# Optimization experiments

Hardware: AMD Instinct MI355X
Metric: run time of the kernel (lower is better)

## Reference

```python
import jax, jax.numpy as jnp
import numpy as np

H = 8  # num_heads
EPS = 1e-5

def _layernorm(x, g, b):
    mu = jnp.mean(x, axis=-1, keepdims=True)
    var = jnp.var(x, axis=-1, keepdims=True)
    return (x - mu) * jax.lax.rsqrt(var + EPS) * g + b

def setup_inputs() -> dict:
    key = jax.random.key(0)
    ks = jax.random.split(key, 16)
    B, S, D, F = 1, 4096, 512, 2048
    s = 1.0 / np.sqrt(D)
    inp = {
        'x': jax.random.normal(ks[0], (B, S, D), jnp.float32),
        'mask': jax.random.randint(ks[1], (S, S), 0, 2, jnp.int32),
        'wq': jax.random.normal(ks[2], (D, D), jnp.float32) * s,
        'bq': jnp.zeros((D,), jnp.float32),
        'wk': jax.random.normal(ks[3], (D, D), jnp.float32) * s,
        'bk': jnp.zeros((D,), jnp.float32),
        'wv': jax.random.normal(ks[4], (D, D), jnp.float32) * s,
        'bv': jnp.zeros((D,), jnp.float32),
        'wo': jax.random.normal(ks[5], (D, D), jnp.float32) * s,
        'bo': jnp.zeros((D,), jnp.float32),
        'w1': jax.random.normal(ks[6], (D, F), jnp.float32) * s,
        'b1': jnp.zeros((F,), jnp.float32),
        'w2': jax.random.normal(ks[7], (F, D), jnp.float32) * (1.0 / np.sqrt(F)),
        'b2': jnp.zeros((D,), jnp.float32),
        'g1': jnp.ones((D,), jnp.float32),
        'be1': jnp.zeros((D,), jnp.float32),
        'g2': jnp.ones((D,), jnp.float32),
        'be2': jnp.zeros((D,), jnp.float32),
    }
    return inp

def reference(x, mask, wq, bq, wk, bk, wv, bv, wo, bo, w1, b1, w2, b2, g1, be1, g2, be2):
    B, S, D = x.shape
    Dh = D // H

    def split(t):  # (B,S,D) -> (B,H,S,Dh)
        return t.reshape(B, S, H, Dh).transpose(0, 2, 1, 3)

    q = split(x @ wq + bq)
    k = split(x @ wk + bk)
    v = split(x @ wv + bv)

    # naive attention: full (B,H,S,S) scores, NO 1/sqrt(Dh) scaling (faithful to source)
    scores = jnp.einsum('bhsd,bhtd->bhst', q, k)
    scores = jnp.where(mask == 0, jnp.float32(-1e9), scores)
    attn = jax.nn.softmax(scores, axis=-1)
    out = jnp.einsum('bhst,bhtd->bhsd', attn, v)
    out = out.transpose(0, 2, 1, 3).reshape(B, S, D) @ wo + bo

    x = _layernorm(x + out, g1, be1)  # dropout is identity at inference
    ff = jax.nn.relu(x @ w1 + b1) @ w2 + b2
    x = _layernorm(x + ff, g2, be2)
    return x
```

## Files before the change

kernel.cpp:

```cpp
#include <hip/hip_runtime.h>

typedef unsigned short u16;
typedef unsigned int u32;
typedef unsigned long long u64;
typedef __attribute__((ext_vector_type(4))) float f32x4;
typedef __attribute__((ext_vector_type(8))) short bf16x8;
typedef __attribute__((ext_vector_type(4))) u16 u16x4;
typedef __attribute__((ext_vector_type(2))) u32 u32x2;

#define DEV __device__ __forceinline__

DEV u16 f2bf(float f) {
  union { float f; u32 u; } c; c.f = f;
  u32 u = c.u;
  u += 0x7fffu + ((u >> 16) & 1u);
  return (u16)(u >> 16);
}
DEV float bf2f(u16 h) {
  union { u32 u; float f; } c; c.u = ((u32)h) << 16;
  return c.f;
}
DEV u32 fbits(float f) { union { float f; u32 u; } c; c.f = f; return c.u; }
DEV u32 packtrunc(float a, float b) {
  return (fbits(b) & 0xFFFF0000u) | (fbits(a) >> 16);
}

DEV void gload_lds16(const void* g, void* l) {
  __builtin_amdgcn_global_load_lds(
      (const __attribute__((address_space(1))) u32*)(u64)g,
      (__attribute__((address_space(3))) u32*)(u32)(u64)l,
      16, 0, 0);
}

struct PrepW { const float* w; u16* th; u16* tl; int R, C, gxmask, gxshift; };
struct PrepArgs {
  const float* x; u16* xh; u16* xl;
  const int* mask; unsigned long long* mbits;
  PrepW pw[6];
};

__global__ __launch_bounds__(256) void prep(PrepArgs a) {
  __shared__ float t[32][33];
  int b = blockIdx.x, tid = threadIdx.x;
  if (b < 2048) {
    int i = (b * 256 + tid) * 4;
    f32x4 v = *(const f32x4*)(a.x + i);
    u16x4 h, l;
#pragma unroll
    for (int j = 0; j < 4; ++j) { h[j] = f2bf(v[j]); l[j] = f2bf(v[j] - bf2f(h[j])); }
    *(u16x4*)(a.xh + i) = h;
    *(u16x4*)(a.xl + i) = l;
    return;
  }
  b -= 2048;
  if (b < 3072) {
    int wi, base;
    if (b < 1024) { wi = b >> 8; base = b & 255; }
    else if (b < 2048) { wi = 4; base = b - 1024; }
    else { wi = 5; base = b - 2048; }
    PrepW p = a.pw[wi];
    int c0 = (base & p.gxmask) * 32, r0 = (base >> p.gxshift) * 32;
    int tx = tid & 31, ty = tid >> 5;
#pragma unroll
    for (int i = 0; i < 4; ++i)
      t[ty + 8 * i][tx] = p.w[(size_t)(r0 + ty + 8 * i) * p.C + c0 + tx];
    __syncthreads();
#pragma unroll
    for (int i = 0; i < 4; ++i) {
      float v = t[tx][ty + 8 * i];
      u16 h = f2bf(v);
      size_t o = (size_t)(c0 + ty + 8 * i) * p.R + r0 + tx;
      p.th[o] = h;
      p.tl[o] = f2bf(v - bf2f(h));
    }
    return;
  }
  b -= 3072;
  size_t i = (size_t)b * 256 + tid;
  unsigned long long bb = __ballot(a.mask[i] != 0);
  if ((tid & 63) == 0) a.mbits[i >> 6] = bb;
}

struct QkvArgs {
  const u16 *Ah, *Al;
  const u16 *Bh[3], *Bl[3];
  const float* bias[3];
  u16 *Qh, *Ql, *Kh, *Vt;
};

__global__ __launch_bounds__(256) void gemm_qkv(QkvArgs a) {
  const int K = 512;
  const float L2E = 1.44269504088896340736f;
  const int z = blockIdx.z;
  const u16* __restrict__ Bh = a.Bh[z];
  const u16* __restrict__ Bl = a.Bl[z];
  const float* __restrict__ bias = a.bias[z];
  const int bn = blockIdx.x * 128, bm = blockIdx.y * 128;
  const int tid = threadIdx.x;
  const int wave = tid >> 6, lane = tid & 63;
  const int l16 = lane & 15, quad = lane >> 4;
  const int wm = (wave >> 1) * 64, wn = (wave & 1) * 64;

  __shared__ u16 sA[128 * 32];
  __shared__ u16 sB[128 * 32];
  __shared__ u16 sAl[128 * 32];
  __shared__ u16 sBl[128 * 32];

  const int srow = wave * 32 + (lane >> 2);
  const int scol = (lane & 3) * 8;
  const u16* srcA0 = a.Ah + (size_t)(bm + srow) * K + scol;
  const u16* srcB0 = Bh + (size_t)(bn + srow) * K + scol;
  const u16* srcAl0 = a.Al + (size_t)(bm + srow) * K + scol;
  const u16* srcBl0 = Bl + (size_t)(bn + srow) * K + scol;
  const size_t half_off = (size_t)16 * K;
  u16* dstA = sA + wave * 1024;
  u16* dstB = sB + wave * 1024;
  u16* dstAl = sAl + wave * 1024;
  u16* dstBl = sBl + wave * 1024;

  f32x4 acc[4][4] = {};

  for (int kt = 0; kt < K; kt += 32) {
    gload_lds16(srcA0 + kt, dstA);
    gload_lds16(srcA0 + half_off + kt, dstA + 512);
    gload_lds16(srcB0 + kt, dstB);
    gload_lds16(srcB0 + half_off + kt, dstB + 512);
    gload_lds16(srcAl0 + kt, dstAl);
    gload_lds16(srcAl0 + half_off + kt, dstAl + 512);
    gload_lds16(srcBl0 + kt, dstBl);
    gload_lds16(srcBl0 + half_off + kt, dstBl + 512);
    __syncthreads();

    bf16x8 a_h[4], b_h[4], a_l[4], b_l[4];
#pragma unroll
    for (int mt = 0; mt < 4; ++mt) {
      a_h[mt] = *(const bf16x8*)(sA + (wm + mt * 16 + l16) * 32 + quad * 8);
      a_l[mt] = *(const bf16x8*)(sAl + (wm + mt * 16 + l16) * 32 + quad * 8);
    }
#pragma unroll
    for (int nt = 0; nt < 4; ++nt) {
      b_h[nt] = *(const bf16x8*)(sB + (wn + nt * 16 + l16) * 32 + quad * 8);
      b_l[nt] = *(const bf16x8*)(sBl + (wn + nt * 16 + l16) * 32 + quad * 8);
    }
#pragma unroll
    for (int mt = 0; mt < 4; ++mt)
#pragma unroll
      for (int nt = 0; nt < 4; ++nt) {
        acc[mt][nt] = __builtin_amdgcn_mfma_f32_16x16x32_bf16(a_h[mt], b_h[nt], acc[mt][nt], 0, 0, 0);
        acc[mt][nt] = __builtin_amdgcn_mfma_f32_16x16x32_bf16(a_h[mt], b_l[nt], acc[mt][nt], 0, 0, 0);
        acc[mt][nt] = __builtin_amdgcn_mfma_f32_16x16x32_bf16(a_l[mt], b_h[nt], acc[mt][nt], 0, 0, 0);
      }
    __syncthreads();
  }

  if (z == 2) {
#pragma unroll
    for (int nt = 0; nt < 4; ++nt) {
      int col = bn + wn + nt * 16 + l16;
      float bv = bias[col];
#pragma unroll
      for (int mt = 0; mt < 4; ++mt) {
        int row0 = bm + wm + mt * 16 + quad * 4;
        u16x4 o;
#pragma unroll
        for (int r = 0; r < 4; ++r) o[r] = f2bf(acc[mt][nt][r] + bv);
        *(u16x4*)(a.Vt + (size_t)col * 4096 + row0) = o;
      }
    }
  } else if (z == 0) {
#pragma unroll
    for (int mt = 0; mt < 4; ++mt)
#pragma unroll
      for (int nt = 0; nt < 4; ++nt) {
        int col = bn + wn + nt * 16 + l16;
        float bv = bias[col];
#pragma unroll
        for (int r = 0; r < 4; ++r) {
          int row = bm + wm + mt * 16 + quad * 4 + r;
          float v = (acc[mt][nt][r] + bv) * L2E;
          u16 h = f2bf(v);
          size_t oidx = (size_t)row * 512 + col;
          a.Qh[oidx] = h;
          a.Ql[oidx] = f2bf(v - bf2f(h));
        }
      }
  } else {
#pragma unroll
    for (int mt = 0; mt < 4; ++mt)
#pragma unroll
      for (int nt = 0; nt < 4; ++nt) {
        int col = bn + wn + nt * 16 + l16;
        float bv = bias[col];
#pragma unroll
        for (int r = 0; r < 4; ++r) {
          int row = bm + wm + mt * 16 + quad * 4 + r;
          a.Kh[(size_t)row * 512 + col] = f2bf(acc[mt][nt][r] + bv);
        }
      }
  }
}

template <int RELU, int BF16OUT>
__global__ __launch_bounds__(256) void gemm_bt(const u16* __restrict__ Ah,
                                               const u16* __restrict__ Bh,
                                               const float* __restrict__ bias,
                                               float* __restrict__ Cf,
                                               u16* __restrict__ Ch,
                                               int N, int K) {
  const int bn = blockIdx.x * 128, bm = blockIdx.y * 128;
  const int tid = threadIdx.x;
  const int wave = tid >> 6, lane = tid & 63;
  const int l16 = lane & 15, quad = lane >> 4;
  const int wm = (wave >> 1) * 64, wn = (wave & 1) * 64;

  __shared__ u16 sA[128 * 32];
  __shared__ u16 sB[128 * 32];

  const int srow = wave * 32 + (lane >> 2);
  const int scol = (lane & 3) * 8;
  const u16* srcA0 = Ah + (size_t)(bm + srow) * K + scol;
  const u16* srcB0 = Bh + (size_t)(bn + srow) * K + scol;
  const size_t half_off = (size_t)16 * K;
  u16* dstA = sA + wave * 1024;
  u16* dstB = sB + wave * 1024;

  f32x4 acc[4][4] = {};

  for (int kt = 0; kt < K; kt += 32) {
    gload_lds16(srcA0 + kt, dstA);
    gload_lds16(srcA0 + half_off + kt, dstA + 512);
    gload_lds16(srcB0 + kt, dstB);
    gload_lds16(srcB0 + half_off + kt, dstB + 512);
    __syncthreads();

    bf16x8 a_h[4], b_h[4];
#pragma unroll
    for (int mt = 0; mt < 4; ++mt)
      a_h[mt] = *(const bf16x8*)(sA + (wm + mt * 16 + l16) * 32 + quad * 8);
#pragma unroll
    for (int nt = 0; nt < 4; ++nt)
      b_h[nt] = *(const bf16x8*)(sB + (wn + nt * 16 + l16) * 32 + quad * 8);
#pragma unroll
    for (int mt = 0; mt < 4; ++mt)
#pragma unroll
      for (int nt = 0; nt < 4; ++nt)
        acc[mt][nt] = __builtin_amdgcn_mfma_f32_16x16x32_bf16(a_h[mt], b_h[nt], acc[mt][nt], 0, 0, 0);
    __syncthreads();
  }

#pragma unroll
  for (int mt = 0; mt < 4; ++mt)
#pragma unroll
    for (int nt = 0; nt < 4; ++nt) {
      int col = bn + wn + nt * 16 + l16;
      float bv = bias ? bias[col] : 0.f;
#pragma unroll
      for (int r = 0; r < 4; ++r) {
        int row = bm + wm + mt * 16 + quad * 4 + r;
        float v = acc[mt][nt][r] + bv;
        if (RELU) v = fmaxf(v, 0.f);
        size_t oidx = (size_t)row * N + col;
        if (BF16OUT) Ch[oidx] = f2bf(v);
        else Cf[oidx] = v;
      }
    }
}

__global__ __launch_bounds__(256) void attn(const u16* __restrict__ Qh, const u16* __restrict__ Ql,
                                            const u16* __restrict__ Kh, const u16* __restrict__ Vt,
                                            const u64* __restrict__ mb64,
                                            float* __restrict__ O0, float* __restrict__ O1,
                                            float* __restrict__ O2, float* __restrict__ O3,
                                            float* __restrict__ lp) {
  const int S = 4096, D = 512;
  const int h = blockIdx.x >> 2, chunk = blockIdx.x & 3;
  const int tid = threadIdx.x, wave = tid >> 6, lane = tid & 63;
  const int l16 = lane & 15, quad = lane >> 4;
  const int q0w = blockIdx.y * 128 + wave * 32;
  const int kbeg = chunk * 1024;
  const int sw = l16 & 7;

  __shared__ u16 sK[64 * 64];
  __shared__ u16 sV[80 * 64];
  __shared__ u16 sP[4][32 * 64];
  u16* myP = &sP[wave][0];

  if (tid < 16) ((u64*)(sV + 64 * 64))[tid] = 0x3F803F803F803F80ULL;
  for (int idx = tid; idx < 240; idx += 256) ((u64*)(sV + 65 * 64))[idx] = 0;

  const int skey = lane >> 3;
  const int sch  = lane & 7;
  const u16* srcK = Kh + (size_t)(kbeg + wave * 8 + skey) * D + h * 64 + ((sch ^ skey) * 8);
  const u16* srcV = Vt + (size_t)(h * 64 + wave * 8 + skey) * S + kbeg + ((sch ^ skey) * 8);
  u16* dstK = sK + wave * 512;
  u16* dstV = sV + wave * 512;

  bf16x8 qfh[2][2], qfl[2][2];
#pragma unroll
  for (int qt = 0; qt < 2; ++qt)
#pragma unroll
    for (int kd = 0; kd < 2; ++kd) {
      size_t qb = (size_t)(q0w + qt * 16 + l16) * D + h * 64 + kd * 32 + quad * 8;
      qfh[qt][kd] = *(const bf16x8*)(Qh + qb);
      qfl[qt][kd] = *(const bf16x8*)(Ql + qb);
    }

  f32x4 accO[2][5] = {};
  const int wbase = kbeg >> 6;

  for (int it = 0; it < 16; ++it) {
    gload_lds16(srcK, dstK);
    gload_lds16(srcK + (size_t)32 * D, dstK + 32 * 64);
    gload_lds16(srcV, dstV);
    gload_lds16(srcV + (size_t)32 * S, dstV + 32 * 64);
    srcK += (size_t)64 * D; srcV += 64;
    __syncthreads();

    u64 wm[2];
#pragma unroll
    for (int qt = 0; qt < 2; ++qt)
      wm[qt] = mb64[(size_t)(q0w + qt * 16 + l16) * 64 + wbase + it];

#pragma unroll
    for (int half = 0; half < 2; ++half) {
      f32x4 sc[2][2];
#pragma unroll
      for (int k2 = 0; k2 < 2; ++k2) {
        const int kt4 = half * 2 + k2;
        const u16* arow = sK + (kt4 * 16 + l16) * 64;
        bf16x8 ka0 = *(const bf16x8*)(arow + ((quad ^ sw) * 8));
        bf16x8 ka1 = *(const bf16x8*)(arow + (((4 + quad) ^ sw) * 8));
#pragma unroll
        for (int qt = 0; qt < 2; ++qt) {
          f32x4 s = {};
          s = __builtin_amdgcn_mfma_f32_16x16x32_bf16(ka0, qfh[qt][0], s, 0, 0, 0);
          s = __builtin_amdgcn_mfma_f32_16x16x32_bf16(ka1, qfh[qt][1], s, 0, 0, 0);
          s = __builtin_amdgcn_mfma_f32_16x16x32_bf16(ka0, qfl[qt][0], s, 0, 0, 0);
          s = __builtin_amdgcn_mfma_f32_16x16x32_bf16(ka1, qfl[qt][1], s, 0, 0, 0);
          sc[k2][qt] = s;
        }
      }
#pragma unroll
      for (int k2 = 0; k2 < 2; ++k2) {
        const int kt4 = half * 2 + k2;
        const int baseb = (kt4 & 1) * 16 + quad * 4;
#pragma unroll
        for (int qt = 0; qt < 2; ++qt) {
          u32 wbits = half ? (u32)(wm[qt] >> 32) : (u32)wm[qt];
          float p[4];
#pragma unroll
          for (int r = 0; r < 4; ++r) {
            bool keep = (wbits >> (baseb + r)) & 1u;
            p[r] = exp2f(keep ? sc[k2][qt][r] : -1e9f);
          }
          int row = qt * 16 + l16;
          int pos = (kt4 * 2 + (quad >> 1)) ^ sw;
          u32x2 pk = {packtrunc(p[0], p[1]), packtrunc(p[2], p[3])};
          *(u32x2*)(myP + row * 64 + pos * 8 + (quad & 1) * 4) = pk;
        }
      }
    }
#pragma unroll
    for (int kt2 = 0; kt2 < 2; ++kt2) {
      bf16x8 pa[2];
#pragma unroll
      for (int qt = 0; qt < 2; ++qt)
        pa[qt] = *(const bf16x8*)(myP + (qt * 16 + l16) * 64 + (((kt2 * 4 + quad) ^ sw) * 8));
#pragma unroll
      for (int nt = 0; nt < 5; ++nt) {
        bf16x8 vf = *(const bf16x8*)(sV + (nt * 16 + l16) * 64 + (((kt2 * 4 + quad) ^ sw) * 8));
#pragma unroll
        for (int qt = 0; qt < 2; ++qt)
          accO[qt][nt] = __builtin_amdgcn_mfma_f32_16x16x32_bf16(pa[qt], vf, accO[qt][nt], 0, 0, 0);
      }
    }
    __syncthreads();
  }

  float* Op = (chunk < 2) ? (chunk ? O1 : O0) : (chunk == 2 ? O2 : O3);
#pragma unroll
  for (int qt = 0; qt < 2; ++qt)
#pragma unroll
    for (int nt = 0; nt < 4; ++nt)
#pragma unroll
      for (int r = 0; r < 4; ++r) {
        int row = q0w + qt * 16 + quad * 4 + r;
        Op[((size_t)h * S + row) * 64 + nt * 16 + l16] = accO[qt][nt][r];
      }
  if (l16 == 0)
#pragma unroll
    for (int qt = 0; qt < 2; ++qt)
#pragma unroll
      for (int r = 0; r < 4; ++r)
        lp[((size_t)h * 4 + chunk) * S + q0w + qt * 16 + quad * 4 + r] = accO[qt][4][r];
}

__global__ __launch_bounds__(256) void attn_combine(const float* __restrict__ O0,
                                                    const float* __restrict__ O1,
                                                    const float* __restrict__ O2,
                                                    const float* __restrict__ O3,
                                                    const float* __restrict__ lp,
                                                    u16* __restrict__ ctx) {
  const int S = 4096;
  int i = (blockIdx.x * 256 + threadIdx.x);
  int row = i >> 7;
  int col4 = (i & 127) * 4;
  int h = col4 >> 6, c = col4 & 63;
  size_t ob = ((size_t)h * S + row) * 64 + c;
  f32x4 o = *(const f32x4*)(O0 + ob) + *(const f32x4*)(O1 + ob) +
            *(const f32x4*)(O2 + ob) + *(const f32x4*)(O3 + ob);
  float l = lp[((size_t)h * 4 + 0) * S + row] + lp[((size_t)h * 4 + 1) * S + row] +
            lp[((size_t)h * 4 + 2) * S + row] + lp[((size_t)h * 4 + 3) * S + row];
  float rl = 1.f / l;
  u16x4 out;
#pragma unroll
  for (int j = 0; j < 4; ++j) out[j] = f2bf(o[j] * rl);
  *(u16x4*)(ctx + (size_t)row * 512 + col4) = out;
}

__global__ __launch_bounds__(256) void resid_ln(const float* __restrict__ X,
                                                const float* __restrict__ Y,
                                                const float* __restrict__ g,
                                                const float* __restrict__ b,
                                                float* __restrict__ outF,
                                                u16* __restrict__ outH) {
  int row = blockIdx.x * 4 + (int)(threadIdx.x >> 6);
  int lane = threadIdx.x & 63;
  const float* x0 = X + (size_t)row * 512;
  const float* y0 = Y + (size_t)row * 512;
  int c0 = lane * 4, c1 = 256 + lane * 4;
  f32x4 v0 = *(const f32x4*)(x0 + c0) + *(const f32x4*)(y0 + c0);
  f32x4 v1 = *(const f32x4*)(x0 + c1) + *(const f32x4*)(y0 + c1);
  float s = 0.f, s2 = 0.f;
#pragma unroll
  for (int j = 0; j < 4; ++j) {
    s += v0[j] + v1[j];
    s2 += v0[j] * v0[j] + v1[j] * v1[j];
  }
#pragma unroll
  for (int m = 1; m < 64; m <<= 1) {
    s += __shfl_xor(s, m);
    s2 += __shfl_xor(s2, m);
  }
  float mean = s * (1.f / 512.f);
  float var = s2 * (1.f / 512.f) - mean * mean;
  float rs = rsqrtf(var + 1e-5f);
  f32x4 o0, o1;
#pragma unroll
  for (int j = 0; j < 4; ++j) {
    o0[j] = (v0[j] - mean) * rs * g[c0 + j] + b[c0 + j];
    o1[j] = (v1[j] - mean) * rs * g[c1 + j] + b[c1 + j];
  }
  if (outF) {
    *(f32x4*)(outF + (size_t)row * 512 + c0) = o0;
    *(f32x4*)(outF + (size_t)row * 512 + c1) = o1;
  }
  if (outH) {
    u16x4 h0, h1;
#pragma unroll
    for (int j = 0; j < 4; ++j) { h0[j] = f2bf(o0[j]); h1[j] = f2bf(o1[j]); }
    *(u16x4*)(outH + (size_t)row * 512 + c0) = h0;
    *(u16x4*)(outH + (size_t)row * 512 + c1) = h1;
  }
}

extern "C" void kernel_launch(void* const* d_in, const int* in_sizes, int n_in,
                              void* d_out, int out_size, void* d_ws, size_t ws_size,
                              hipStream_t stream) {
  (void)in_sizes; (void)n_in; (void)out_size; (void)ws_size;
  const float* x   = (const float*)d_in[0];
  const int*   mask= (const int*)d_in[1];
  const float* wq  = (const float*)d_in[2];
  const float* bq  = (const float*)d_in[3];
  const float* wk  = (const float*)d_in[4];
  const float* bk  = (const float*)d_in[5];
  const float* wv  = (const float*)d_in[6];
  const float* bv  = (const float*)d_in[7];
  const float* wo  = (const float*)d_in[8];
  const float* bo  = (const float*)d_in[9];
  const float* w1  = (const float*)d_in[10];
  const float* b1  = (const float*)d_in[11];
  const float* w2  = (const float*)d_in[12];
  const float* b2  = (const float*)d_in[13];
  const float* g1  = (const float*)d_in[14];
  const float* be1 = (const float*)d_in[15];
  const float* g2  = (const float*)d_in[16];
  const float* be2 = (const float*)d_in[17];

  const int S = 4096, D = 512, F = 2048;
  char* ws = (char*)d_ws;
  size_t cur = 0;
  auto alloc = [&](size_t bytes) {
    char* p = ws + cur;
    cur += (bytes + 255) & ~(size_t)255;
    return p;
  };
  u16* wqT_h = (u16*)alloc((size_t)D * D * 2); u16* wqT_l = (u16*)alloc((size_t)D * D * 2);
  u16* wkT_h = (u16*)alloc((size_t)D * D * 2); u16* wkT_l = (u16*)alloc((size_t)D * D * 2);
  u16* wvT_h = (u16*)alloc((size_t)D * D * 2); u16* wvT_l = (u16*)alloc((size_t)D * D * 2);
  u16* woT_h = (u16*)alloc((size_t)D * D * 2); u16* woT_l = (u16*)alloc((size_t)D * D * 2);
  u16* w1T_h = (u16*)alloc((size_t)D * F * 2); u16* w1T_l = (u16*)alloc((size_t)D * F * 2);
  u16* w2T_h = (u16*)alloc((size_t)D * F * 2); u16* w2T_l = (u16*)alloc((size_t)D * F * 2);
  u32* mbits = (u32*)alloc((size_t)S * S / 8);
  u16* xh = (u16*)alloc((size_t)S * D * 2);
  u16* xl = (u16*)alloc((size_t)S * D * 2);
  u16* Qh = (u16*)alloc((size_t)S * D * 2);
  u16* Ql = (u16*)alloc((size_t)S * D * 2);
  u16* Kh = (u16*)alloc((size_t)S * D * 2);
  u16* Vt = (u16*)alloc((size_t)S * D * 2);
  u16* ctx = (u16*)alloc((size_t)S * D * 2);
  float* x1 = (float*)alloc((size_t)S * D * 4);
  u16* x1h = (u16*)alloc((size_t)S * D * 2);
  float* Oex = (float*)alloc((size_t)2 * S * D * 4);
  float* O0 = (float*)xh;
  float* O1 = x1;
  float* O2 = Oex;
  float* O3 = Oex + (size_t)S * D;
  float* lp = (float*)x1h;
  float* proj = (float*)xh;
  u16* hbuf = Qh;
  float* ff2 = Oex;

  PrepArgs pa;
  pa.x = x; pa.xh = xh; pa.xl = xl;
  pa.mask = mask; pa.mbits = (unsigned long long*)mbits;
  pa.pw[0] = {wq, wqT_h, wqT_l, D, D, 15, 4};
  pa.pw[1] = {wk, wkT_h, wkT_l, D, D, 15, 4};
  pa.pw[2] = {wv, wvT_h, wvT_l, D, D, 15, 4};
  pa.pw[3] = {wo, woT_h, woT_l, D, D, 15, 4};
  pa.pw[4] = {w1, w1T_h, w1T_l, D, F, 63, 6};
  pa.pw[5] = {w2, w2T_h, w2T_l, F, D, 15, 4};

  QkvArgs qa;
  qa.Ah = xh; qa.Al = xl;
  qa.Bh[0] = wqT_h; qa.Bh[1] = wkT_h; qa.Bh[2] = wvT_h;
  qa.Bl[0] = wqT_l; qa.Bl[1] = wkT_l; qa.Bl[2] = wvT_l;
  qa.bias[0] = bq; qa.bias[1] = bk; qa.bias[2] = bv;
  qa.Qh = Qh; qa.Ql = Ql; qa.Kh = Kh; qa.Vt = Vt;

  prep<<<70656, 256, 0, stream>>>(pa);
  gemm_qkv<<<dim3(4, 32, 3), 256, 0, stream>>>(qa);
  attn<<<dim3(32, 32), 256, 0, stream>>>(Qh, Ql, Kh, Vt, (const u64*)mbits, O0, O1, O2, O3, lp);
  attn_combine<<<(S * D / 4) / 256, 256, 0, stream>>>(O0, O1, O2, O3, lp, ctx);
  gemm_bt<0, 0><<<dim3(4, 32), 256, 0, stream>>>(ctx, woT_h, bo, proj, nullptr, D, D);
  resid_ln<<<S / 4, 256, 0, stream>>>(x, proj, g1, be1, x1, x1h);
  gemm_bt<1, 1><<<dim3(16, 32), 256, 0, stream>>>(x1h, w1T_h, b1, nullptr, hbuf, F, D);
  gemm_bt<0, 0><<<dim3(4, 32), 256, 0, stream>>>(hbuf, w2T_h, b2, ff2, nullptr, D, F);
  resid_ln<<<S / 4, 256, 0, stream>>>(x1, ff2, g2, be2, (float*)d_out, nullptr);
}
```

Before: 370.8 us.

## Drop Q low-part, split attention keys 8-way, split-K GEMMs with double buffering

```diff
diff --git a/kernel.cpp b/kernel.cpp
--- a/kernel.cpp
+++ b/kernel.cpp
@@ -71,7 +71,7 @@
       u16 h = f2bf(v);
       size_t o = (size_t)(c0 + ty + 8 * i) * p.R + r0 + tx;
       p.th[o] = h;
-      p.tl[o] = f2bf(v - bf2f(h));
+      if (p.tl) p.tl[o] = f2bf(v - bf2f(h));
     }
     return;
   }
@@ -85,7 +85,7 @@
   const u16 *Ah, *Al;
   const u16 *Bh[3], *Bl[3];
   const float* bias[3];
-  u16 *Qh, *Ql, *Kh, *Vt;
+  u16 *Qh, *Kh, *Vt;
 };
 
 __global__ __launch_bounds__(256) void gemm_qkv(QkvArgs a) {
@@ -167,7 +167,9 @@
         *(u16x4*)(a.Vt + (size_t)col * 4096 + row0) = o;
       }
     }
-  } else if (z == 0) {
+  } else {
+    u16* __restrict__ C = (z == 0) ? a.Qh : a.Kh;
+    float scale = (z == 0) ? L2E : 1.f;
 #pragma unroll
     for (int mt = 0; mt < 4; ++mt)
 #pragma unroll
@@ -177,30 +179,13 @@
 #pragma unroll
         for (int r = 0; r < 4; ++r) {
           int row = bm + wm + mt * 16 + quad * 4 + r;
-          float v = (acc[mt][nt][r] + bv) * L2E;
-          u16 h = f2bf(v);
-          size_t oidx = (size_t)row * 512 + col;
-          a.Qh[oidx] = h;
-          a.Ql[oidx] = f2bf(v - bf2f(h));
+          C[(size_t)row * 512 + col] = f2bf((acc[mt][nt][r] + bv) * scale);
         }
       }
-  } else {
-#pragma unroll
-    for (int mt = 0; mt < 4; ++mt)
-#pragma unroll
-      for (int nt = 0; nt < 4; ++nt) {
-        int col = bn + wn + nt * 16 + l16;
-        float bv = bias[col];
-#pragma unroll
-        for (int r = 0; r < 4; ++r) {
-          int row = bm + wm + mt * 16 + quad * 4 + r;
-          a.Kh[(size_t)row * 512 + col] = f2bf(acc[mt][nt][r] + bv);
-        }
-      }
-  }
-}
-
-template <int RELU, int BF16OUT>
+  }
+}
+
+template <int RELU, int BF16OUT, int NSPLIT>
 __global__ __launch_bounds__(256) void gemm_bt(const u16* __restrict__ Ah,
                                                const u16* __restrict__ Bh,
                                                const float* __restrict__ bias,
@@ -208,44 +193,52 @@
                                                u16* __restrict__ Ch,
                                                int N, int K) {
   const int bn = blockIdx.x * 128, bm = blockIdx.y * 128;
+  const int kbeg = blockIdx.z * (K / NSPLIT);
   const int tid = threadIdx.x;
   const int wave = tid >> 6, lane = tid & 63;
   const int l16 = lane & 15, quad = lane >> 4;
   const int wm = (wave >> 1) * 64, wn = (wave & 1) * 64;
 
-  __shared__ u16 sA[128 * 32];
-  __shared__ u16 sB[128 * 32];
+  __shared__ u16 sA[2][128 * 32];
+  __shared__ u16 sB[2][128 * 32];
 
   const int srow = wave * 32 + (lane >> 2);
   const int scol = (lane & 3) * 8;
-  const u16* srcA0 = Ah + (size_t)(bm + srow) * K + scol;
-  const u16* srcB0 = Bh + (size_t)(bn + srow) * K + scol;
+  const u16* srcA0 = Ah + (size_t)(bm + srow) * K + kbeg + scol;
+  const u16* srcB0 = Bh + (size_t)(bn + srow) * K + kbeg + scol;
   const size_t half_off = (size_t)16 * K;
-  u16* dstA = sA + wave * 1024;
-  u16* dstB = sB + wave * 1024;
+
+  auto prefetchG = [&](int kt, int buf) {
+    u16* dA = sA[buf] + wave * 1024;
+    u16* dB = sB[buf] + wave * 1024;
+    gload_lds16(srcA0 + kt, dA);
+    gload_lds16(srcA0 + half_off + kt, dA + 512);
+    gload_lds16(srcB0 + kt, dB);
+    gload_lds16(srcB0 + half_off + kt, dB + 512);
+  };
 
   f32x4 acc[4][4] = {};
-
-  for (int kt = 0; kt < K; kt += 32) {
-    gload_lds16(srcA0 + kt, dstA);
-    gload_lds16(srcA0 + half_off + kt, dstA + 512);
-    gload_lds16(srcB0 + kt, dstB);
-    gload_lds16(srcB0 + half_off + kt, dstB + 512);
+  prefetchG(0, 0);
+
+  const int steps = (K / NSPLIT) >> 5;
+  for (int i = 0; i < steps; ++i) {
     __syncthreads();
+    if (i + 1 < steps) prefetchG((i + 1) << 5, (i + 1) & 1);
+    const u16* bufA = sA[i & 1];
+    const u16* bufB = sB[i & 1];
 
     bf16x8 a_h[4], b_h[4];
 #pragma unroll
     for (int mt = 0; mt < 4; ++mt)
-      a_h[mt] = *(const bf16x8*)(sA + (wm + mt * 16 + l16) * 32 + quad * 8);
+      a_h[mt] = *(const bf16x8*)(bufA + (wm + mt * 16 + l16) * 32 + quad * 8);
 #pragma unroll
     for (int nt = 0; nt < 4; ++nt)
-      b_h[nt] = *(const bf16x8*)(sB + (wn + nt * 16 + l16) * 32 + quad * 8);
+      b_h[nt] = *(const bf16x8*)(bufB + (wn + nt * 16 + l16) * 32 + quad * 8);
 #pragma unroll
     for (int mt = 0; mt < 4; ++mt)
 #pragma unroll
       for (int nt = 0; nt < 4; ++nt)
         acc[mt][nt] = __builtin_amdgcn_mfma_f32_16x16x32_bf16(a_h[mt], b_h[nt], acc[mt][nt], 0, 0, 0);
-    __syncthreads();
   }
 
 #pragma unroll
@@ -253,40 +246,42 @@
 #pragma unroll
     for (int nt = 0; nt < 4; ++nt) {
       int col = bn + wn + nt * 16 + l16;
-      float bv = bias ? bias[col] : 0.f;
+      float bv = (bias && (NSPLIT == 1 || blockIdx.z == 0)) ? bias[col] : 0.f;
 #pragma unroll
       for (int r = 0; r < 4; ++r) {
         int row = bm + wm + mt * 16 + quad * 4 + r;
         float v = acc[mt][nt][r] + bv;
-        if (RELU) v = fmaxf(v, 0.f);
         size_t oidx = (size_t)row * N + col;
-        if (BF16OUT) Ch[oidx] = f2bf(v);
-        else Cf[oidx] = v;
+        if (NSPLIT == 1) {
+          if (RELU) v = fmaxf(v, 0.f);
+          if (BF16OUT) Ch[oidx] = f2bf(v);
+          else Cf[oidx] = v;
+        } else {
+          atomicAdd(&Cf[oidx], v);
+        }
       }
     }
 }
 
-__global__ __launch_bounds__(256) void attn(const u16* __restrict__ Qh, const u16* __restrict__ Ql,
-                                            const u16* __restrict__ Kh, const u16* __restrict__ Vt,
-                                            const u64* __restrict__ mb64,
-                                            float* __restrict__ O0, float* __restrict__ O1,
-                                            float* __restrict__ O2, float* __restrict__ O3,
-                                            float* __restrict__ lp) {
+struct AttnIO { float* O[8]; float* lp; };
+
+__global__ __launch_bounds__(256, 6) void attn(const u16* __restrict__ Qh,
+                                               const u16* __restrict__ Kh,
+                                               const u16* __restrict__ Vt,
+                                               const u64* __restrict__ mb64,
+                                               AttnIO io) {
   const int S = 4096, D = 512;
-  const int h = blockIdx.x >> 2, chunk = blockIdx.x & 3;
+  const int h = blockIdx.x >> 3, chunk = blockIdx.x & 7;
   const int tid = threadIdx.x, wave = tid >> 6, lane = tid & 63;
   const int l16 = lane & 15, quad = lane >> 4;
   const int q0w = blockIdx.y * 128 + wave * 32;
-  const int kbeg = chunk * 1024;
+  const int kbeg = chunk * 512;
   const int sw = l16 & 7;
 
   __shared__ u16 sK[64 * 64];
-  __shared__ u16 sV[80 * 64];
-  __shared__ u16 sP[4][32 * 64];
+  __shared__ u16 sV[64 * 64];
+  __shared__ u16 sP[4][32 * 40];
   u16* myP = &sP[wave][0];
-
-  if (tid < 16) ((u64*)(sV + 64 * 64))[tid] = 0x3F803F803F803F80ULL;
-  for (int idx = tid; idx < 240; idx += 256) ((u64*)(sV + 65 * 64))[idx] = 0;
 
   const int skey = lane >> 3;
   const int sch  = lane & 7;
@@ -295,20 +290,18 @@
   u16* dstK = sK + wave * 512;
   u16* dstV = sV + wave * 512;
 
-  bf16x8 qfh[2][2], qfl[2][2];
+  bf16x8 qf[2][2];
 #pragma unroll
   for (int qt = 0; qt < 2; ++qt)
 #pragma unroll
-    for (int kd = 0; kd < 2; ++kd) {
-      size_t qb = (size_t)(q0w + qt * 16 + l16) * D + h * 64 + kd * 32 + quad * 8;
-      qfh[qt][kd] = *(const bf16x8*)(Qh + qb);
-      qfl[qt][kd] = *(const bf16x8*)(Ql + qb);
-    }
-
-  f32x4 accO[2][5] = {};
+    for (int kd = 0; kd < 2; ++kd)
+      qf[qt][kd] = *(const bf16x8*)(Qh + (size_t)(q0w + qt * 16 + l16) * D + h * 64 + kd * 32 + quad * 8);
+
+  f32x4 accO[2][4] = {};
+  float l_lane[2] = {0.f, 0.f};
   const int wbase = kbeg >> 6;
 
-  for (int it = 0; it < 16; ++it) {
+  for (int it = 0; it < 8; ++it) {
     gload_lds16(srcK, dstK);
     gload_lds16(srcK + (size_t)32 * D, dstK + 32 * 64);
     gload_lds16(srcV, dstV);
@@ -333,42 +326,34 @@
 #pragma unroll
         for (int qt = 0; qt < 2; ++qt) {
           f32x4 s = {};
-          s = __builtin_amdgcn_mfma_f32_16x16x32_bf16(ka0, qfh[qt][0], s, 0, 0, 0);
-          s = __builtin_amdgcn_mfma_f32_16x16x32_bf16(ka1, qfh[qt][1], s, 0, 0, 0);
-          s = __builtin_amdgcn_mfma_f32_16x16x32_bf16(ka0, qfl[qt][0], s, 0, 0, 0);
-          s = __builtin_amdgcn_mfma_f32_16x16x32_bf16(ka1, qfl[qt][1], s, 0, 0, 0);
+          s = __builtin_amdgcn_mfma_f32_16x16x32_bf16(ka0, qf[qt][0], s, 0, 0, 0);
+          s = __builtin_amdgcn_mfma_f32_16x16x32_bf16(ka1, qf[qt][1], s, 0, 0, 0);
           sc[k2][qt] = s;
         }
       }
 #pragma unroll
       for (int k2 = 0; k2 < 2; ++k2) {
-        const int kt4 = half * 2 + k2;
-        const int baseb = (kt4 & 1) * 16 + quad * 4;
+        const int baseb = half * 32 + k2 * 16 + quad * 4;
 #pragma unroll
         for (int qt = 0; qt < 2; ++qt) {
-          u32 wbits = half ? (u32)(wm[qt] >> 32) : (u32)wm[qt];
           float p[4];
 #pragma unroll
           for (int r = 0; r < 4; ++r) {
-            bool keep = (wbits >> (baseb + r)) & 1u;
+            bool keep = (wm[qt] >> (baseb + r)) & 1ull;
             p[r] = exp2f(keep ? sc[k2][qt][r] : -1e9f);
           }
-          int row = qt * 16 + l16;
-          int pos = (kt4 * 2 + (quad >> 1)) ^ sw;
+          l_lane[qt] += (p[0] + p[1]) + (p[2] + p[3]);
           u32x2 pk = {packtrunc(p[0], p[1]), packtrunc(p[2], p[3])};
-          *(u32x2*)(myP + row * 64 + pos * 8 + (quad & 1) * 4) = pk;
+          *(u32x2*)(myP + (qt * 16 + l16) * 40 + k2 * 16 + quad * 4) = pk;
         }
       }
-    }
-#pragma unroll
-    for (int kt2 = 0; kt2 < 2; ++kt2) {
       bf16x8 pa[2];
 #pragma unroll
       for (int qt = 0; qt < 2; ++qt)
-        pa[qt] = *(const bf16x8*)(myP + (qt * 16 + l16) * 64 + (((kt2 * 4 + quad) ^ sw) * 8));
-#pragma unroll
-      for (int nt = 0; nt < 5; ++nt) {
-        bf16x8 vf = *(const bf16x8*)(sV + (nt * 16 + l16) * 64 + (((kt2 * 4 + quad) ^ sw) * 8));
+        pa[qt] = *(const bf16x8*)(myP + (qt * 16 + l16) * 40 + quad * 8);
+#pragma unroll
+      for (int nt = 0; nt < 4; ++nt) {
+        bf16x8 vf = *(const bf16x8*)(sV + (nt * 16 + l16) * 64 + (((half * 4 + quad) ^ sw) * 8));
 #pragma unroll
         for (int qt = 0; qt < 2; ++qt)
           accO[qt][nt] = __builtin_amdgcn_mfma_f32_16x16x32_bf16(pa[qt], vf, accO[qt][nt], 0, 0, 0);
@@ -377,7 +362,14 @@
     __syncthreads();
   }
 
-  float* Op = (chunk < 2) ? (chunk ? O1 : O0) : (chunk == 2 ? O2 : O3);
+#pragma unroll
+  for (int qt = 0; qt < 2; ++qt) {
+    float s = l_lane[qt];
+    s += __shfl_xor(s, 16);
+    s += __shfl_xor(s, 32);
+    l_lane[qt] = s;
+  }
+  float* Op = io.O[chunk];
 #pragma unroll
   for (int qt = 0; qt < 2; ++qt)
 #pragma unroll
@@ -387,35 +379,34 @@
         int row = q0w + qt * 16 + quad * 4 + r;
         Op[((size_t)h * S + row) * 64 + nt * 16 + l16] = accO[qt][nt][r];
       }
-  if (l16 == 0)
+  if (quad == 0)
 #pragma unroll
     for (int qt = 0; qt < 2; ++qt)
-#pragma unroll
-      for (int r = 0; r < 4; ++r)
-        lp[((size_t)h * 4 + chunk) * S + q0w + qt * 16 + quad * 4 + r] = accO[qt][4][r];
-}
-
-__global__ __launch_bounds__(256) void attn_combine(const float* __restrict__ O0,
-                                                    const float* __restrict__ O1,
-                                                    const float* __restrict__ O2,
-                                                    const float* __restrict__ O3,
-                                                    const float* __restrict__ lp,
-                                                    u16* __restrict__ ctx) {
+      io.lp[((size_t)h * 8 + chunk) * S + q0w + qt * 16 + l16] = l_lane[qt];
+}
+
+__global__ __launch_bounds__(256) void attn_combine(AttnIO io, u16* __restrict__ ctx) {
   const int S = 4096;
   int i = (blockIdx.x * 256 + threadIdx.x);
   int row = i >> 7;
   int col4 = (i & 127) * 4;
   int h = col4 >> 6, c = col4 & 63;
   size_t ob = ((size_t)h * S + row) * 64 + c;
-  f32x4 o = *(const f32x4*)(O0 + ob) + *(const f32x4*)(O1 + ob) +
-            *(const f32x4*)(O2 + ob) + *(const f32x4*)(O3 + ob);
-  float l = lp[((size_t)h * 4 + 0) * S + row] + lp[((size_t)h * 4 + 1) * S + row] +
-            lp[((size_t)h * 4 + 2) * S + row] + lp[((size_t)h * 4 + 3) * S + row];
+  f32x4 o = {0.f, 0.f, 0.f, 0.f};
+  float l = 0.f;
+#pragma unroll
+  for (int p = 0; p < 8; ++p) {
+    o += *(const f32x4*)(io.O[p] + ob);
+    l += io.lp[((size_t)h * 8 + p) * S + row];
+  }
   float rl = 1.f / l;
   u16x4 out;
 #pragma unroll
   for (int j = 0; j < 4; ++j) out[j] = f2bf(o[j] * rl);
   *(u16x4*)(ctx + (size_t)row * 512 + col4) = out;
+  f32x4 z = {0.f, 0.f, 0.f, 0.f};
+  *(f32x4*)(io.O[0] + ob) = z;
+  *(f32x4*)(io.O[2] + ob) = z;
 }
 
 __global__ __launch_bounds__(256) void resid_ln(const float* __restrict__ X,
@@ -498,25 +489,25 @@
   u16* wqT_h = (u16*)alloc((size_t)D * D * 2); u16* wqT_l = (u16*)alloc((size_t)D * D * 2);
   u16* wkT_h = (u16*)alloc((size_t)D * D * 2); u16* wkT_l = (u16*)alloc((size_t)D * D * 2);
   u16* wvT_h = (u16*)alloc((size_t)D * D * 2); u16* wvT_l = (u16*)alloc((size_t)D * D * 2);
-  u16* woT_h = (u16*)alloc((size_t)D * D * 2); u16* woT_l = (u16*)alloc((size_t)D * D * 2);
-  u16* w1T_h = (u16*)alloc((size_t)D * F * 2); u16* w1T_l = (u16*)alloc((size_t)D * F * 2);
-  u16* w2T_h = (u16*)alloc((size_t)D * F * 2); u16* w2T_l = (u16*)alloc((size_t)D * F * 2);
+  u16* woT_h = (u16*)alloc((size_t)D * D * 2);
+  u16* w1T_h = (u16*)alloc((size_t)D * F * 2);
+  u16* w2T_h = (u16*)alloc((size_t)D * F * 2);
   u32* mbits = (u32*)alloc((size_t)S * S / 8);
   u16* xh = (u16*)alloc((size_t)S * D * 2);
   u16* xl = (u16*)alloc((size_t)S * D * 2);
   u16* Qh = (u16*)alloc((size_t)S * D * 2);
-  u16* Ql = (u16*)alloc((size_t)S * D * 2);
   u16* Kh = (u16*)alloc((size_t)S * D * 2);
   u16* Vt = (u16*)alloc((size_t)S * D * 2);
+  u16* hx = (u16*)alloc((size_t)S * D * 2);
   u16* ctx = (u16*)alloc((size_t)S * D * 2);
   float* x1 = (float*)alloc((size_t)S * D * 4);
   u16* x1h = (u16*)alloc((size_t)S * D * 2);
-  float* Oex = (float*)alloc((size_t)2 * S * D * 4);
-  float* O0 = (float*)xh;
-  float* O1 = x1;
-  float* O2 = Oex;
-  float* O3 = Oex + (size_t)S * D;
-  float* lp = (float*)x1h;
+  float* Oex = (float*)alloc((size_t)6 * S * D * 4);
+  AttnIO io;
+  io.O[0] = (float*)xh;
+  io.O[1] = x1;
+  for (int p = 2; p < 8; ++p) io.O[p] = Oex + (size_t)(p - 2) * S * D;
+  io.lp = (float*)x1h;
   float* proj = (float*)xh;
   u16* hbuf = Qh;
   float* ff2 = Oex;
@@ -527,24 +518,24 @@
   pa.pw[0] = {wq, wqT_h, wqT_l, D, D, 15, 4};
   pa.pw[1] = {wk, wkT_h, wkT_l, D, D, 15, 4};
   pa.pw[2] = {wv, wvT_h, wvT_l, D, D, 15, 4};
-  pa.pw[3] = {wo, woT_h, woT_l, D, D, 15, 4};
-  pa.pw[4] = {w1, w1T_h, w1T_l, D, F, 63, 6};
-  pa.pw[5] = {w2, w2T_h, w2T_l, F, D, 15, 4};
+  pa.pw[3] = {wo, woT_h, nullptr, D, D, 15, 4};
+  pa.pw[4] = {w1, w1T_h, nullptr, D, F, 63, 6};
+  pa.pw[5] = {w2, w2T_h, nullptr, F, D, 15, 4};
 
   QkvArgs qa;
   qa.Ah = xh; qa.Al = xl;
   qa.Bh[0] = wqT_h; qa.Bh[1] = wkT_h; qa.Bh[2] = wvT_h;
   qa.Bl[0] = wqT_l; qa.Bl[1] = wkT_l; qa.Bl[2] = wvT_l;
   qa.bias[0] = bq; qa.bias[1] = bk; qa.bias[2] = bv;
-  qa.Qh = Qh; qa.Ql = Ql; qa.Kh = Kh; qa.Vt = Vt;
+  qa.Qh = Qh; qa.Kh = Kh; qa.Vt = Vt;
 
   prep<<<70656, 256, 0, stream>>>(pa);
   gemm_qkv<<<dim3(4, 32, 3), 256, 0, stream>>>(qa);
-  attn<<<dim3(32, 32), 256, 0, stream>>>(Qh, Ql, Kh, Vt, (const u64*)mbits, O0, O1, O2, O3, lp);
-  attn_combine<<<(S * D / 4) / 256, 256, 0, stream>>>(O0, O1, O2, O3, lp, ctx);
-  gemm_bt<0, 0><<<dim3(4, 32), 256, 0, stream>>>(ctx, woT_h, bo, proj, nullptr, D, D);
+  attn<<<dim3(64, 32), 256, 0, stream>>>(Qh, Kh, Vt, (const u64*)mbits, io);
+  attn_combine<<<(S * D / 4) / 256, 256, 0, stream>>>(io, ctx);
+  gemm_bt<0, 0, 4><<<dim3(4, 32, 4), 256, 0, stream>>>(ctx, woT_h, bo, proj, nullptr, D, D);
   resid_ln<<<S / 4, 256, 0, stream>>>(x, proj, g1, be1, x1, x1h);
-  gemm_bt<1, 1><<<dim3(16, 32), 256, 0, stream>>>(x1h, w1T_h, b1, nullptr, hbuf, F, D);
-  gemm_bt<0, 0><<<dim3(4, 32), 256, 0, stream>>>(hbuf, w2T_h, b2, ff2, nullptr, D, F);
+  gemm_bt<1, 1, 1><<<dim3(16, 32, 1), 256, 0, stream>>>(x1h, w1T_h, b1, nullptr, hbuf, F, D);
+  gemm_bt<0, 0, 4><<<dim3(4, 32, 4), 256, 0, stream>>>(hbuf, w2T_h, b2, ff2, nullptr, D, F);
   resid_ln<<<S / 4, 256, 0, stream>>>(x1, ff2, g2, be2, (float*)d_out, nullptr);
 }
```

Result: slower. 642.7 us (+73.3%).
